# Kernel tuning notes

Measured on AMD Instinct MI355X. Metric: run time of the kernel, lower is better.

The kernel has to match this reference:

```python
import jax, jax.numpy as jnp
import numpy as np

SP = 4          # window/split size
HEADS = 8       # num_heads
SHIFTS = (0, 2) # shift_sizes


def _rel_pos_index(sp):
    # Same construction as the torch buffer `relative_position_index`.
    coords = np.stack(np.meshgrid(np.arange(sp), np.arange(sp), indexing='ij'))  # [2,sp,sp]
    coords = coords.reshape(2, -1)                                               # [2, sp*sp]
    rel = coords[:, :, None] - coords[:, None, :]                                # [2, N, N]
    rel = rel.transpose(1, 2, 0).astype(np.int64)                                # [N, N, 2]
    rel[..., 0] += sp - 1
    rel[..., 1] += sp - 1
    rel[..., 0] *= 2 * sp - 1
    return rel.sum(-1)  # [N, N]


def _window_attend(xh, qkv_w, lepe_w, bias, sp, heads, scale):
    # xh: [B, c, H, W] with c = split_dim
    B, c, H, W = xh.shape
    hd = c // heads
    h, w = H // sp, W // sp
    # 1x1 conv to qkv (no bias)
    qkv = jnp.einsum('oi,bihw->bohw', qkv_w, xh)
    q, k, v = jnp.split(qkv, 3, axis=1)
    # depthwise 3x3 LePE on v
    lepe = jax.lax.conv_general_dilated(v, lepe_w, (1, 1), 'SAME',
                                        feature_group_count=c)

    def part(t):
        # 'b (c head) (h hsp) (w wsp) -> (b h w) head (hsp wsp) c'
        t = t.reshape(B, hd, heads, h, sp, w, sp)
        t = t.transpose(0, 3, 5, 2, 4, 6, 1)  # b,h,w,head,hsp,wsp,hd
        return t.reshape(B * h * w, heads, sp * sp, hd)

    q, k, v, lepe = map(part, (q, k, v, lepe))
    attn = jnp.einsum('nhqc,nhkc->nhqk', q * scale, k) + bias[None]  # [N,heads,16,16]
    attn = jax.nn.softmax(attn, axis=-1)
    out = jnp.einsum('nhqk,nhkc->nhqc', attn, v) + lepe
    # inverse rearrange back to [B, c, H, W]
    out = out.reshape(B, h, w, heads, sp, sp, hd)
    out = out.transpose(0, 6, 3, 1, 4, 2, 5).reshape(B, c, H, W)
    return out


def setup_inputs() -> dict:
    key = jax.random.key(0)
    k1, k2, k3, k4 = jax.random.split(key, 4)
    x = jax.random.normal(k1, (8, 128, 192, 192), dtype=jnp.float32)
    qkv_w = jax.random.normal(k2, (192, 64), dtype=jnp.float32) * 0.05   # [3*split_dim, split_dim]
    lepe_w = jax.random.normal(k3, (64, 1, 3, 3), dtype=jnp.float32) * 0.05  # depthwise
    bias_table = jax.random.normal(k4, (49, 8), dtype=jnp.float32) * 0.02    # [(2sp-1)^2, heads]
    return {'x': x, 'qkv_w': qkv_w, 'lepe_w': lepe_w, 'bias_table': bias_table}


def reference(x, qkv_w, lepe_w, bias_table):
    B, C, H, W = x.shape
    c = C // 2
    hd = c // HEADS
    scale = hd ** -0.5
    idx = _rel_pos_index(SP)  # static numpy [16,16]
    bias = bias_table[idx.reshape(-1)].reshape(SP * SP, SP * SP, HEADS)
    bias = bias.transpose(2, 0, 1)  # [heads, 16, 16]

    results = []
    for s in SHIFTS:
        # NOTE: faithful to source, roll is over dims (1,2) = (channel, height)
        xs = jnp.roll(x, (-s, -s), axis=(1, 2)) if s > 0 else x
        halves = (xs[:, :c], xs[:, c:])
        outs = [_window_attend(xh, qkv_w, lepe_w, bias, SP, HEADS, scale)
                for xh in halves]
        if s > 0:
            outs = [jnp.roll(o, (s, s), axis=(1, 2)) for o in outs]
        results.append(jnp.concatenate(outs, axis=1))
    return results[0] + results[1]
```

## Files before the change

kernel.cpp:

```cpp
#include <hip/hip_runtime.h>

typedef __attribute__((ext_vector_type(8))) short short8v;
typedef __attribute__((ext_vector_type(8))) __fp16 h8v;
typedef __attribute__((ext_vector_type(2))) __fp16 h2v;
typedef __attribute__((ext_vector_type(4))) float f32x4;

__device__ inline unsigned short f2bf(float f) {
    unsigned u = __builtin_bit_cast(unsigned, f);
    return (unsigned short)((u + 0x7FFFu + ((u >> 16) & 1u)) >> 16);
}

__device__ inline float dot2(h2v a, h2v b, float c) {
#if __has_builtin(__builtin_amdgcn_fdot2)
    return __builtin_amdgcn_fdot2(a, b, c, false);
#else
    return c + (float)a[0] * (float)b[0] + (float)a[1] * (float)b[1];
#endif
}
__device__ inline h2v pk2h(float a, float b) {
#if __has_builtin(__builtin_amdgcn_cvt_pkrtz)
    return __builtin_bit_cast(h2v, __builtin_amdgcn_cvt_pkrtz(a, b));
#else
    h2v r; r[0] = (__fp16)a; r[1] = (__fp16)b; return r;
#endif
}

__global__ __launch_bounds__(256) void prep_weights(const float* __restrict__ qkv_w,
                                                    __fp16* __restrict__ wf) {
    int it = blockIdx.x * 256 + threadIdx.x;
    if (it >= 1536) return;
    int l = it & 63, frag = it >> 6;
    int which = frag >> 3, nt = (frag >> 1) & 3, kst = frag & 1;
    const float* src = qkv_w + (which * 64 + nt * 16 + (l & 15)) * 64 + kst * 32 + (l >> 4) * 8;
    h8v pk;
    #pragma unroll
    for (int j = 0; j < 8; ++j) pk[j] = (__fp16)src[j];
    *reinterpret_cast<h8v*>(wf + it * 8) = pk;
}

__global__ __launch_bounds__(256) void prep_x(const float* __restrict__ x,
                                              __fp16* __restrict__ xh) {
    const int xt = blockIdx.x;
    const int y  = blockIdx.y;
    const int b  = blockIdx.z;
    const int x0 = xt * 32;
    __shared__ float buf[128 * 33];

    for (int it = threadIdx.x; it < 1024; it += 256) {
        int c = it >> 3, xq = it & 7;
        const float4 v = *reinterpret_cast<const float4*>(
            x + ((b * 128 + c) * 192 + y) * 192 + x0 + xq * 4);
        float* d = &buf[c * 33 + xq * 4];
        d[0] = v.x; d[1] = v.y; d[2] = v.z; d[3] = v.w;
    }
    __syncthreads();

    for (int it = threadIdx.x; it < 512; it += 256) {
        int xl = it >> 4, c8 = it & 15;
        h8v pk;
        #pragma unroll
        for (int j = 0; j < 8; ++j) pk[j] = (__fp16)buf[(c8 * 8 + j) * 33 + xl];
        __fp16* dst = xh + (((size_t)(b * 192 + y) * 192) + x0 + xl) * 130 + c8 * 8;
        __builtin_memcpy(dst, &pk, 16);
    }
    if (threadIdx.x < 32) {
        int xl = threadIdx.x;
        h2v d2; d2[0] = (__fp16)buf[0 * 33 + xl]; d2[1] = (__fp16)buf[1 * 33 + xl];
        __fp16* dst = xh + (((size_t)(b * 192 + y) * 192) + x0 + xl) * 130 + 128;
        __builtin_memcpy(dst, &d2, 4);
    }
}

template<int SHIFT, bool ACCUM>
__global__ __launch_bounds__(256) void swin_main(
    const __fp16* __restrict__ xh,
    const __fp16* __restrict__ wfrag,
    const float* __restrict__ lepe_w,
    const float* __restrict__ bias_table,
    float* __restrict__ out)
{
    const int bx = blockIdx.x;
    const int wy = bx / 12, strip = bx % 12;
    const int half = blockIdx.y, b = blockIdx.z;
    const int tid = threadIdx.x;
    const int w = tid >> 6, l = tid & 63;

    __shared__ __fp16 xv[108 * 64];
    __shared__ __fp16 qs[64 * 64];
    __shared__ __fp16 ks[64 * 64];
    __shared__ __fp16 bias_s[392];
    __shared__ __fp16 lepe_s[576];

    for (int i = tid; i < 392; i += 256) bias_s[i] = (__fp16)bias_table[i];
    for (int i = tid; i < 576; i += 256) {
        int d = i & 7, rest = i >> 3;
        int j = rest % 9, h = rest / 9;
        lepe_s[i] = (__fp16)lepe_w[(d * 8 + h) * 9 + j];
    }

    const int ry0 = wy * 4 - 1, rx0 = strip * 16 - 1;
    for (int it = tid; it < 864; it += 256) {
        const int pos = it >> 3, slot = it & 7;
        const int py = pos / 18, px = pos - py * 18;
        const int ry = ry0 + py, rx = rx0 + px;
        h8v val;
        #pragma unroll
        for (int j = 0; j < 8; ++j) val[j] = (__fp16)0.f;
        if (ry >= 0 && ry < 192 && rx >= 0 && rx < 192) {
            int phys = ry + SHIFT; if (phys >= 192) phys -= 192;
            const int srcslot = slot ^ (pos & 7);
            const __fp16* src = xh + (((size_t)(b * 192 + phys) * 192) + rx) * 130
                                   + half * 64 + srcslot * 8 + SHIFT;
            __builtin_memcpy(&val, src, 16);
        }
        *reinterpret_cast<h8v*>(&xv[pos * 64 + slot * 8]) = val;
    }
    __syncthreads();

    const int tok16 = l & 15, g = l >> 4;
    h8v Aq[2], Av[3][2];
    {
        const int posq = (1 + (tok16 >> 2)) * 18 + w * 4 + 1 + (tok16 & 3);
        #pragma unroll
        for (int kst = 0; kst < 2; ++kst) {
            int chunk = (kst * 4 + g) ^ (posq & 7);
            Aq[kst] = *reinterpret_cast<const h8v*>(&xv[posq * 64 + chunk * 8]);
        }
        #pragma unroll
        for (int mt = 0; mt < 3; ++mt) {
            int t = mt * 16 + tok16;
            int posv = (t < 36) ? ((t / 6) * 18 + w * 4 + (t % 6)) : 0;
            #pragma unroll
            for (int kst = 0; kst < 2; ++kst) {
                int chunk = (kst * 4 + g) ^ (posv & 7);
                Av[mt][kst] = *reinterpret_cast<const h8v*>(&xv[posv * 64 + chunk * 8]);
            }
        }
    }
    __syncthreads();

    #pragma unroll
    for (int nt = 0; nt < 4; ++nt) {
        h8v Bq[2], Bk[2], Bv[2];
        #pragma unroll
        for (int kst = 0; kst < 2; ++kst) {
            Bq[kst] = *reinterpret_cast<const h8v*>(wfrag + (((0 * 8 + nt * 2 + kst) * 64 + l) * 8));
            Bk[kst] = *reinterpret_cast<const h8v*>(wfrag + (((1 * 8 + nt * 2 + kst) * 64 + l) * 8));
            Bv[kst] = *reinterpret_cast<const h8v*>(wfrag + (((2 * 8 + nt * 2 + kst) * 64 + l) * 8));
        }
        f32x4 aQ = {0.f,0.f,0.f,0.f}, aK = {0.f,0.f,0.f,0.f};
        f32x4 aV[3];
        #pragma unroll
        for (int mt = 0; mt < 3; ++mt) aV[mt] = (f32x4){0.f,0.f,0.f,0.f};
        #pragma unroll
        for (int kst = 0; kst < 2; ++kst) {
            aQ = __builtin_amdgcn_mfma_f32_16x16x32_f16(Aq[kst], Bq[kst], aQ, 0, 0, 0);
            aK = __builtin_amdgcn_mfma_f32_16x16x32_f16(Aq[kst], Bk[kst], aK, 0, 0, 0);
            #pragma unroll
            for (int mt = 0; mt < 3; ++mt)
                aV[mt] = __builtin_amdgcn_mfma_f32_16x16x32_f16(Av[mt][kst], Bv[kst], aV[mt], 0, 0, 0);
        }
        const int ch  = nt * 16 + tok16;
        const int chp = (ch & 7) * 8 + (ch >> 3);
        #pragma unroll
        for (int r = 0; r < 4; ++r) {
            const int qtok = w * 16 + 4 * g + r;
            const int pb = (((chp >> 3) ^ (qtok & 7)) * 8 + (chp & 7));
            qs[qtok * 64 + pb] = (__fp16)(aQ[r] * 0.35355339059327373f);
            ks[qtok * 64 + pb] = (__fp16)aK[r];
        }
        #pragma unroll
        for (int mt = 0; mt < 3; ++mt)
            #pragma unroll
            for (int r = 0; r < 4; ++r) {
                int t = mt * 16 + 4 * g + r;
                if (t < 36) {
                    int py = t / 6, px = t - py * 6;
                    int pos = py * 18 + w * 4 + px;
                    int pb = (((chp >> 3) ^ (pos & 7)) * 8 + (chp & 7));
                    xv[pos * 64 + pb] = (__fp16)aV[mt][r];
                }
            }
    }
    __syncthreads();

    {
        const int h = l >> 3, tqp = l & 7;
        const int qy0 = tqp >> 2, qx0 = tqp & 3;

        const int ox = strip * 16 + w * 4 + qx0;
        int oy0 = wy * 4 + qy0 + SHIFT;     if (oy0 >= 192) oy0 -= 192;
        int oy1 = wy * 4 + qy0 + 2 + SHIFT; if (oy1 >= 192) oy1 -= 192;
        int idx0[8], idx1[8];
        float prev0[8], prev1[8];
        #pragma unroll
        for (int d = 0; d < 8; ++d) {
            const int oc = half * 64 + ((d * 8 + h + SHIFT) & 63);
            idx0[d] = ((b * 128 + oc) * 192 + oy0) * 192 + ox;
            idx1[d] = ((b * 128 + oc) * 192 + oy1) * 192 + ox;
            if (ACCUM) { prev0[d] = out[idx0[d]]; prev1[d] = out[idx1[d]]; }
        }

        const int t0 = w * 16 + tqp, t1 = t0 + 8;
        h8v q0 = *reinterpret_cast<const h8v*>(&qs[t0 * 64 + (h ^ (t0 & 7)) * 8]);
        h8v q1 = *reinterpret_cast<const h8v*>(&qs[t1 * 64 + (h ^ (t1 & 7)) * 8]);
        const h2v* q0p = reinterpret_cast<const h2v*>(&q0);
        const h2v* q1p = reinterpret_cast<const h2v*>(&q1);

        float sc0[16], sc1[16];
        float den0 = 0.f, den1 = 0.f;
        #pragma unroll
        for (int tk = 0; tk < 16; ++tk) {
            const int kt = w * 16 + tk;
            h8v kr = *reinterpret_cast<const h8v*>(&ks[kt * 64 + (h ^ (kt & 7)) * 8]);
            const h2v* kp = reinterpret_cast<const h2v*>(&kr);
            float s0 = 0.f, s1 = 0.f;
            #pragma unroll
            for (int i = 0; i < 4; ++i) { s0 = dot2(q0p[i], kp[i], s0); s1 = dot2(q1p[i], kp[i], s1); }
            const int ky = tk >> 2, kx = tk & 3;
            s0 += (float)bias_s[((qy0 - ky + 3) * 7 + (qx0 - kx + 3)) * 8 + h];
            s1 += (float)bias_s[((qy0 + 2 - ky + 3) * 7 + (qx0 - kx + 3)) * 8 + h];
            s0 = __expf(s0); s1 = __expf(s1);
            sc0[tk] = s0; sc1[tk] = s1;
            den0 += s0; den1 += s1;
        }
        const float inv0 = 1.f / den0, inv1 = 1.f / den1;

        h2v o0pk[4], o1pk[4];
        #pragma unroll
        for (int j = 0; j < 4; ++j) { o0pk[j] = pk2h(0.f, 0.f); o1pk[j] = pk2h(0.f, 0.f); }
        #pragma unroll
        for (int tk = 0; tk < 16; ++tk) {
            const int pos = (1 + (tk >> 2)) * 18 + w * 4 + 1 + (tk & 3);
            h8v vr = *reinterpret_cast<const h8v*>(&xv[pos * 64 + (h ^ (pos & 7)) * 8]);
            const h2v* vp = reinterpret_cast<const h2v*>(&vr);
            const float f0 = sc0[tk] * inv0, f1 = sc1[tk] * inv1;
            const h2v pb0 = pk2h(f0, f0), pb1 = pk2h(f1, f1);
            #pragma unroll
            for (int j = 0; j < 4; ++j) {
                o0pk[j] += pb0 * vp[j];
                o1pk[j] += pb1 * vp[j];
            }
        }

        #pragma unroll
        for (int dy = 0; dy < 3; ++dy)
            #pragma unroll
            for (int dx = 0; dx < 3; ++dx) {
                int p0i = (qy0 + dy) * 18 + w * 4 + qx0 + dx;
                int p1i = p0i + 36;
                h8v v0 = *reinterpret_cast<const h8v*>(&xv[p0i * 64 + (h ^ (p0i & 7)) * 8]);
                h8v v1 = *reinterpret_cast<const h8v*>(&xv[p1i * 64 + (h ^ (p1i & 7)) * 8]);
                h8v lw = *reinterpret_cast<const h8v*>(&lepe_s[(h * 9 + dy * 3 + dx) * 8]);
                const h2v* v0p = reinterpret_cast<const h2v*>(&v0);
                const h2v* v1p = reinterpret_cast<const h2v*>(&v1);
                const h2v* lwp = reinterpret_cast<const h2v*>(&lw);
                #pragma unroll
                for (int j = 0; j < 4; ++j) {
                    o0pk[j] += v0p[j] * lwp[j];
                    o1pk[j] += v1p[j] * lwp[j];
                }
            }

        #pragma unroll
        for (int d = 0; d < 8; ++d) {
            const float a0 = (float)o0pk[d >> 1][d & 1];
            const float a1 = (float)o1pk[d >> 1][d & 1];
            if (ACCUM) { out[idx0[d]] = prev0[d] + a0; out[idx1[d]] = prev1[d] + a1; }
            else       { out[idx0[d]] = a0;            out[idx1[d]] = a1; }
        }
    }
}

template<int SHIFT, bool ACCUM>
__global__ __launch_bounds__(256) void swin_fb(
    const float* __restrict__ x, const float* __restrict__ qkv_w,
    const float* __restrict__ lepe_w, const float* __restrict__ bias_table,
    float* __restrict__ out)
{
    const int C = 128, HH = 192, WW = 192;
    const int win = blockIdx.x, wy = win / 48, wx = win % 48;
    const int half = blockIdx.y, b = blockIdx.z, tid = threadIdx.x;
    __shared__ short xpA[8 * 64 * 8];
    __shared__ float vs[64 * 37], qsf[64 * 17], ksf[64 * 17];
    __shared__ float bias_s[392], lepe_s[576];
    const int ys0 = wy * 4, xs0 = wx * 4;
    for (int i = tid; i < 392; i += 256) bias_s[i] = bias_table[i];
    for (int i = tid; i < 576; i += 256) lepe_s[i] = lepe_w[i];
    for (int item = tid; item < 512; item += 256) {
        const int slot = item >> 6, l = item & 63, kst = slot & 1;
        int p = 0; bool tvalid = true;
        if (slot < 6) { int t48 = (slot >> 1) * 16 + (l & 15); tvalid = (t48 < 36); p = t48; }
        else { int ti = l & 15; p = (1 + (ti >> 2)) * 6 + 1 + (ti & 3); }
        const int c0 = kst * 32 + (l >> 4) * 8;
        short8v pk;
        #pragma unroll
        for (int j = 0; j < 8; ++j) pk[j] = 0;
        if (tvalid) {
            int py = p / 6, px = p - py * 6;
            int ry = ys0 - 1 + py, rx = xs0 - 1 + px;
            if (ry >= 0 && ry < HH && rx >= 0 && rx < WW) {
                int oy = ry + SHIFT; if (oy >= HH) oy -= HH;
                #pragma unroll
                for (int j = 0; j < 8; ++j) {
                    int oc = half * 64 + c0 + j + SHIFT; if (oc >= C) oc -= C;
                    pk[j] = (short)f2bf(x[((b * C + oc) * HH + oy) * WW + rx]);
                }
            }
        }
        *reinterpret_cast<short8v*>(&xpA[item * 8]) = pk;
    }
    const int w = tid >> 6, l = tid & 63, nn = l & 15, g = l >> 4;
    short8v Bq[2], Bk[2], Bv[2];
    #pragma unroll
    for (int kst = 0; kst < 2; ++kst) {
        const int coff = kst * 32 + g * 8;
        const float* s0 = qkv_w + (w * 16 + nn) * 64 + coff;
        const float* s1 = qkv_w + (64 + w * 16 + nn) * 64 + coff;
        const float* s2 = qkv_w + (128 + w * 16 + nn) * 64 + coff;
        short8v p0, p1, p2;
        #pragma unroll
        for (int j = 0; j < 8; ++j) { p0[j] = (short)f2bf(s0[j]); p1[j] = (short)f2bf(s1[j]); p2[j] = (short)f2bf(s2[j]); }
        Bq[kst] = p0; Bk[kst] = p1; Bv[kst] = p2;
    }
    __syncthreads();
    {
        short8v Aq[2], Avf[3][2];
        #pragma unroll
        for (int kst = 0; kst < 2; ++kst)
            Aq[kst] = *reinterpret_cast<const short8v*>(&xpA[((6 + kst) * 64 + l) * 8]);
        #pragma unroll
        for (int mt = 0; mt < 3; ++mt)
            #pragma unroll
            for (int kst = 0; kst < 2; ++kst)
                Avf[mt][kst] = *reinterpret_cast<const short8v*>(&xpA[((mt * 2 + kst) * 64 + l) * 8]);
        f32x4 aQ = {0,0,0,0}, aK = {0,0,0,0}; f32x4 aV[3];
        #pragma unroll
        for (int mt = 0; mt < 3; ++mt) aV[mt] = (f32x4){0,0,0,0};
        #pragma unroll
        for (int kst = 0; kst < 2; ++kst) {
            aQ = __builtin_amdgcn_mfma_f32_16x16x32_bf16(Aq[kst], Bq[kst], aQ, 0, 0, 0);
            aK = __builtin_amdgcn_mfma_f32_16x16x32_bf16(Aq[kst], Bk[kst], aK, 0, 0, 0);
            #pragma unroll
            for (int mt = 0; mt < 3; ++mt)
                aV[mt] = __builtin_amdgcn_mfma_f32_16x16x32_bf16(Avf[mt][kst], Bv[kst], aV[mt], 0, 0, 0);
        }
        const int ch = w * 16 + nn;
        #pragma unroll
        for (int r = 0; r < 4; ++r) { qsf[ch * 17 + g * 4 + r] = aQ[r]; ksf[ch * 17 + g * 4 + r] = aK[r]; }
        #pragma unroll
        for (int mt = 0; mt < 3; ++mt)
            #pragma unroll
            for (int r = 0; r < 4; ++r) { int tok = mt * 16 + g * 4 + r; if (tok < 36) vs[ch * 37 + tok] = aV[mt][r]; }
    }
    __syncthreads();
    {
        const int tq = tid & 15, h = (tid >> 4) & 7, dh = tid >> 7;
        const int qy = tq >> 2, qx = tq & 3;
        const float scale = 0.35355339059327373f;
        float qreg[8];
        #pragma unroll
        for (int d = 0; d < 8; ++d) qreg[d] = qsf[(d * 8 + h) * 17 + tq] * scale;
        float sc[16]; float m = -1e30f;
        #pragma unroll
        for (int tk = 0; tk < 16; ++tk) {
            float s = 0.f;
            #pragma unroll
            for (int d = 0; d < 8; ++d) s += qreg[d] * ksf[(d * 8 + h) * 17 + tk];
            s += bias_s[((qy - (tk >> 2) + 3) * 7 + (qx - (tk & 3) + 3)) * 8 + h];
            sc[tk] = s; m = fmaxf(m, s);
        }
        float den = 0.f;
        #pragma unroll
        for (int tk = 0; tk < 16; ++tk) { sc[tk] = __expf(sc[tk] - m); den += sc[tk]; }
        const float inv = 1.f / den;
        float lw[4][9];
        #pragma unroll
        for (int dd = 0; dd < 4; ++dd) {
            int ch = (dh * 4 + dd) * 8 + h;
            #pragma unroll
            for (int j = 0; j < 9; ++j) lw[dd][j] = lepe_s[ch * 9 + j];
        }
        float o[4] = {0,0,0,0};
        #pragma unroll
        for (int tk = 0; tk < 16; ++tk) {
            int p = (1 + (tk >> 2)) * 6 + 1 + (tk & 3); float s = sc[tk];
            #pragma unroll
            for (int dd = 0; dd < 4; ++dd) o[dd] += s * vs[((dh * 4 + dd) * 8 + h) * 37 + p];
        }
        int oy = ys0 + qy + SHIFT; if (oy >= HH) oy -= HH;
        const int irx = xs0 + qx;
        #pragma unroll
        for (int dd = 0; dd < 4; ++dd) {
            const int ch = (dh * 4 + dd) * 8 + h;
            float val = o[dd] * inv;
            #pragma unroll
            for (int dy = 0; dy < 3; ++dy)
                #pragma unroll
                for (int dx = 0; dx < 3; ++dx)
                    val += vs[ch * 37 + (qy + dy) * 6 + (qx + dx)] * lw[dd][dy * 3 + dx];
            const int oc = half * 64 + ((ch + SHIFT) & 63);
            const int oidx = ((b * C + oc) * HH + oy) * WW + irx;
            if (ACCUM) out[oidx] += val; else out[oidx] = val;
        }
    }
}

extern "C" void kernel_launch(void* const* d_in, const int* in_sizes, int n_in,
                              void* d_out, int out_size, void* d_ws, size_t ws_size,
                              hipStream_t stream) {
    const float* x          = (const float*)d_in[0];
    const float* qkv_w      = (const float*)d_in[1];
    const float* lepe_w     = (const float*)d_in[2];
    const float* bias_table = (const float*)d_in[3];
    float* out = (float*)d_out;

    const size_t XH_BYTES = 8UL * 192 * 192 * 130 * 2;
    const size_t NEED = 32768 + XH_BYTES;

    if (ws_size >= NEED) {
        __fp16* wf = (__fp16*)d_ws;
        __fp16* xh = (__fp16*)((char*)d_ws + 32768);
        prep_weights<<<6, 256, 0, stream>>>(qkv_w, wf);
        prep_x<<<dim3(6, 192, 8), 256, 0, stream>>>(x, xh);
        dim3 grid(576, 2, 8);
        swin_main<0, false><<<grid, 256, 0, stream>>>(xh, wf, lepe_w, bias_table, out);
        swin_main<2, true ><<<grid, 256, 0, stream>>>(xh, wf, lepe_w, bias_table, out);
    } else {
        dim3 grid(48 * 48, 2, 8);
        swin_fb<0, false><<<grid, 256, 0, stream>>>(x, qkv_w, lepe_w, bias_table, out);
        swin_fb<2, true ><<<grid, 256, 0, stream>>>(x, qkv_w, lepe_w, bias_table, out);
    }
}
```

Baseline: 334.0 us.

## Pad fp16 staging stride, use exp2 softmax with packed scores, and relayout V pool

```diff
diff --git a/kernel.cpp b/kernel.cpp
--- a/kernel.cpp
+++ b/kernel.cpp
@@ -4,6 +4,8 @@
 typedef __attribute__((ext_vector_type(8))) __fp16 h8v;
 typedef __attribute__((ext_vector_type(2))) __fp16 h2v;
 typedef __attribute__((ext_vector_type(4))) float f32x4;
+
+#define XSTRIDE 136
 
 __device__ inline unsigned short f2bf(float f) {
     unsigned u = __builtin_bit_cast(unsigned, f);
@@ -22,6 +24,13 @@
     return __builtin_bit_cast(h2v, __builtin_amdgcn_cvt_pkrtz(a, b));
 #else
     h2v r; r[0] = (__fp16)a; r[1] = (__fp16)b; return r;
+#endif
+}
+__device__ inline float fexp2(float x) {
+#if __has_builtin(__builtin_amdgcn_exp2f)
+    return __builtin_amdgcn_exp2f(x);
+#else
+    return __expf(x * 0.6931471805599453f);
 #endif
 }
 
@@ -60,13 +69,13 @@
         h8v pk;
         #pragma unroll
         for (int j = 0; j < 8; ++j) pk[j] = (__fp16)buf[(c8 * 8 + j) * 33 + xl];
-        __fp16* dst = xh + (((size_t)(b * 192 + y) * 192) + x0 + xl) * 130 + c8 * 8;
+        __fp16* dst = xh + (((size_t)(b * 192 + y) * 192) + x0 + xl) * XSTRIDE + c8 * 8;
         __builtin_memcpy(dst, &pk, 16);
     }
     if (threadIdx.x < 32) {
         int xl = threadIdx.x;
         h2v d2; d2[0] = (__fp16)buf[0 * 33 + xl]; d2[1] = (__fp16)buf[1 * 33 + xl];
-        __fp16* dst = xh + (((size_t)(b * 192 + y) * 192) + x0 + xl) * 130 + 128;
+        __fp16* dst = xh + (((size_t)(b * 192 + y) * 192) + x0 + xl) * XSTRIDE + 128;
         __builtin_memcpy(dst, &d2, 4);
     }
 }
@@ -85,13 +94,13 @@
     const int tid = threadIdx.x;
     const int w = tid >> 6, l = tid & 63;
 
-    __shared__ __fp16 xv[108 * 64];
+    __shared__ __fp16 pool[9216];
     __shared__ __fp16 qs[64 * 64];
     __shared__ __fp16 ks[64 * 64];
-    __shared__ __fp16 bias_s[392];
+    __shared__ float  bias_s[392];
     __shared__ __fp16 lepe_s[576];
 
-    for (int i = tid; i < 392; i += 256) bias_s[i] = (__fp16)bias_table[i];
+    for (int i = tid; i < 392; i += 256) bias_s[i] = bias_table[i] * 1.4426950408889634f;
     for (int i = tid; i < 576; i += 256) {
         int d = i & 7, rest = i >> 3;
         int j = rest % 9, h = rest / 9;
@@ -109,11 +118,11 @@
         if (ry >= 0 && ry < 192 && rx >= 0 && rx < 192) {
             int phys = ry + SHIFT; if (phys >= 192) phys -= 192;
             const int srcslot = slot ^ (pos & 7);
-            const __fp16* src = xh + (((size_t)(b * 192 + phys) * 192) + rx) * 130
+            const __fp16* src = xh + (((size_t)(b * 192 + phys) * 192) + rx) * XSTRIDE
                                    + half * 64 + srcslot * 8 + SHIFT;
             __builtin_memcpy(&val, src, 16);
         }
-        *reinterpret_cast<h8v*>(&xv[pos * 64 + slot * 8]) = val;
+        *reinterpret_cast<h8v*>(&pool[pos * 64 + slot * 8]) = val;
     }
     __syncthreads();
 
@@ -124,7 +133,7 @@
         #pragma unroll
         for (int kst = 0; kst < 2; ++kst) {
             int chunk = (kst * 4 + g) ^ (posq & 7);
-            Aq[kst] = *reinterpret_cast<const h8v*>(&xv[posq * 64 + chunk * 8]);
+            Aq[kst] = *reinterpret_cast<const h8v*>(&pool[posq * 64 + chunk * 8]);
         }
         #pragma unroll
         for (int mt = 0; mt < 3; ++mt) {
@@ -133,7 +142,7 @@
             #pragma unroll
             for (int kst = 0; kst < 2; ++kst) {
                 int chunk = (kst * 4 + g) ^ (posv & 7);
-                Av[mt][kst] = *reinterpret_cast<const h8v*>(&xv[posv * 64 + chunk * 8]);
+                Av[mt][kst] = *reinterpret_cast<const h8v*>(&pool[posv * 64 + chunk * 8]);
             }
         }
     }
@@ -166,19 +175,17 @@
         for (int r = 0; r < 4; ++r) {
             const int qtok = w * 16 + 4 * g + r;
             const int pb = (((chp >> 3) ^ (qtok & 7)) * 8 + (chp & 7));
-            qs[qtok * 64 + pb] = (__fp16)(aQ[r] * 0.35355339059327373f);
+            qs[qtok * 64 + pb] = (__fp16)(aQ[r] * 0.5101293f);
             ks[qtok * 64 + pb] = (__fp16)aK[r];
         }
         #pragma unroll
         for (int mt = 0; mt < 3; ++mt)
             #pragma unroll
             for (int r = 0; r < 4; ++r) {
-                int t = mt * 16 + 4 * g + r;
+                const int t = mt * 16 + 4 * g + r;
                 if (t < 36) {
-                    int py = t / 6, px = t - py * 6;
-                    int pos = py * 18 + w * 4 + px;
-                    int pb = (((chp >> 3) ^ (pos & 7)) * 8 + (chp & 7));
-                    xv[pos * 64 + pb] = (__fp16)aV[mt][r];
+                    const int pb = (((chp >> 3) ^ (t & 7)) * 8 + (chp & 7));
+                    pool[(w * 36 + t) * 64 + pb] = (__fp16)aV[mt][r];
                 }
             }
     }
@@ -187,18 +194,19 @@
     {
         const int h = l >> 3, tqp = l & 7;
         const int qy0 = tqp >> 2, qx0 = tqp & 3;
+        const __fp16* vv = &pool[w * 36 * 64];
 
         const int ox = strip * 16 + w * 4 + qx0;
         int oy0 = wy * 4 + qy0 + SHIFT;     if (oy0 >= 192) oy0 -= 192;
         int oy1 = wy * 4 + qy0 + 2 + SHIFT; if (oy1 >= 192) oy1 -= 192;
-        int idx0[8], idx1[8];
+        const int ddelta = (oy1 - oy0) * 192;
+        int idx0[8];
         float prev0[8], prev1[8];
         #pragma unroll
         for (int d = 0; d < 8; ++d) {
             const int oc = half * 64 + ((d * 8 + h + SHIFT) & 63);
             idx0[d] = ((b * 128 + oc) * 192 + oy0) * 192 + ox;
-            idx1[d] = ((b * 128 + oc) * 192 + oy1) * 192 + ox;
-            if (ACCUM) { prev0[d] = out[idx0[d]]; prev1[d] = out[idx1[d]]; }
+            if (ACCUM) { prev0[d] = out[idx0[d]]; prev1[d] = out[idx0[d] + ddelta]; }
         }
 
         const int t0 = w * 16 + tqp, t1 = t0 + 8;
@@ -207,39 +215,52 @@
         const h2v* q0p = reinterpret_cast<const h2v*>(&q0);
         const h2v* q1p = reinterpret_cast<const h2v*>(&q1);
 
-        float sc0[16], sc1[16];
+        h2v scp0[8], scp1[8];
         float den0 = 0.f, den1 = 0.f;
         #pragma unroll
-        for (int tk = 0; tk < 16; ++tk) {
-            const int kt = w * 16 + tk;
-            h8v kr = *reinterpret_cast<const h8v*>(&ks[kt * 64 + (h ^ (kt & 7)) * 8]);
-            const h2v* kp = reinterpret_cast<const h2v*>(&kr);
-            float s0 = 0.f, s1 = 0.f;
-            #pragma unroll
-            for (int i = 0; i < 4; ++i) { s0 = dot2(q0p[i], kp[i], s0); s1 = dot2(q1p[i], kp[i], s1); }
-            const int ky = tk >> 2, kx = tk & 3;
-            s0 += (float)bias_s[((qy0 - ky + 3) * 7 + (qx0 - kx + 3)) * 8 + h];
-            s1 += (float)bias_s[((qy0 + 2 - ky + 3) * 7 + (qx0 - kx + 3)) * 8 + h];
-            s0 = __expf(s0); s1 = __expf(s1);
-            sc0[tk] = s0; sc1[tk] = s1;
-            den0 += s0; den1 += s1;
+        for (int tkp = 0; tkp < 8; ++tkp) {
+            float e0[2], e1[2];
+            #pragma unroll
+            for (int u = 0; u < 2; ++u) {
+                const int tk = tkp * 2 + u;
+                const int kt = w * 16 + tk;
+                h8v kr = *reinterpret_cast<const h8v*>(&ks[kt * 64 + (h ^ (kt & 7)) * 8]);
+                const h2v* kp = reinterpret_cast<const h2v*>(&kr);
+                float s0 = 0.f, s1 = 0.f;
+                #pragma unroll
+                for (int i = 0; i < 4; ++i) { s0 = dot2(q0p[i], kp[i], s0); s1 = dot2(q1p[i], kp[i], s1); }
+                const int ky = tk >> 2, kx = tk & 3;
+                s0 += bias_s[((qy0 - ky + 3) * 7 + (qx0 - kx + 3)) * 8 + h];
+                s1 += bias_s[((qy0 + 2 - ky + 3) * 7 + (qx0 - kx + 3)) * 8 + h];
+                e0[u] = fexp2(s0); e1[u] = fexp2(s1);
+            }
+            den0 += e0[0] + e0[1]; den1 += e1[0] + e1[1];
+            scp0[tkp] = pk2h(e0[0], e0[1]);
+            scp1[tkp] = pk2h(e1[0], e1[1]);
         }
         const float inv0 = 1.f / den0, inv1 = 1.f / den1;
+        const h2v ip0 = pk2h(inv0, inv0), ip1 = pk2h(inv1, inv1);
 
         h2v o0pk[4], o1pk[4];
         #pragma unroll
         for (int j = 0; j < 4; ++j) { o0pk[j] = pk2h(0.f, 0.f); o1pk[j] = pk2h(0.f, 0.f); }
         #pragma unroll
-        for (int tk = 0; tk < 16; ++tk) {
-            const int pos = (1 + (tk >> 2)) * 18 + w * 4 + 1 + (tk & 3);
-            h8v vr = *reinterpret_cast<const h8v*>(&xv[pos * 64 + (h ^ (pos & 7)) * 8]);
-            const h2v* vp = reinterpret_cast<const h2v*>(&vr);
-            const float f0 = sc0[tk] * inv0, f1 = sc1[tk] * inv1;
-            const h2v pb0 = pk2h(f0, f0), pb1 = pk2h(f1, f1);
-            #pragma unroll
-            for (int j = 0; j < 4; ++j) {
-                o0pk[j] += pb0 * vp[j];
-                o1pk[j] += pb1 * vp[j];
+        for (int tkp = 0; tkp < 8; ++tkp) {
+            const h2v w0 = scp0[tkp] * ip0;
+            const h2v w1 = scp1[tkp] * ip1;
+            #pragma unroll
+            for (int u = 0; u < 2; ++u) {
+                const int tk = tkp * 2 + u;
+                const int t = (1 + (tk >> 2)) * 6 + 1 + (tk & 3);
+                h8v vr = *reinterpret_cast<const h8v*>(&vv[t * 64 + (h ^ (t & 7)) * 8]);
+                const h2v* vp = reinterpret_cast<const h2v*>(&vr);
+                h2v b0; b0[0] = w0[u]; b0[1] = w0[u];
+                h2v b1; b1[0] = w1[u]; b1[1] = w1[u];
+                #pragma unroll
+                for (int j = 0; j < 4; ++j) {
+                    o0pk[j] += b0 * vp[j];
+                    o1pk[j] += b1 * vp[j];
+                }
             }
         }
 
@@ -247,10 +268,10 @@
         for (int dy = 0; dy < 3; ++dy)
             #pragma unroll
             for (int dx = 0; dx < 3; ++dx) {
-                int p0i = (qy0 + dy) * 18 + w * 4 + qx0 + dx;
-                int p1i = p0i + 36;
-                h8v v0 = *reinterpret_cast<const h8v*>(&xv[p0i * 64 + (h ^ (p0i & 7)) * 8]);
-                h8v v1 = *reinterpret_cast<const h8v*>(&xv[p1i * 64 + (h ^ (p1i & 7)) * 8]);
+                const int ta = (qy0 + dy) * 6 + qx0 + dx;
+                const int tb = ta + 12;
+                h8v v0 = *reinterpret_cast<const h8v*>(&vv[ta * 64 + (h ^ (ta & 7)) * 8]);
+                h8v v1 = *reinterpret_cast<const h8v*>(&vv[tb * 64 + (h ^ (tb & 7)) * 8]);
                 h8v lw = *reinterpret_cast<const h8v*>(&lepe_s[(h * 9 + dy * 3 + dx) * 8]);
                 const h2v* v0p = reinterpret_cast<const h2v*>(&v0);
                 const h2v* v1p = reinterpret_cast<const h2v*>(&v1);
@@ -266,8 +287,8 @@
         for (int d = 0; d < 8; ++d) {
             const float a0 = (float)o0pk[d >> 1][d & 1];
             const float a1 = (float)o1pk[d >> 1][d & 1];
-            if (ACCUM) { out[idx0[d]] = prev0[d] + a0; out[idx1[d]] = prev1[d] + a1; }
-            else       { out[idx0[d]] = a0;            out[idx1[d]] = a1; }
+            if (ACCUM) { out[idx0[d]] = prev0[d] + a0; out[idx0[d] + ddelta] = prev1[d] + a1; }
+            else       { out[idx0[d]] = a0;            out[idx0[d] + ddelta] = a1; }
         }
     }
 }
@@ -415,7 +436,7 @@
     const float* bias_table = (const float*)d_in[3];
     float* out = (float*)d_out;
 
-    const size_t XH_BYTES = 8UL * 192 * 192 * 130 * 2;
+    const size_t XH_BYTES = 8UL * 192 * 192 * XSTRIDE * 2;
     const size_t NEED = 32768 + XH_BYTES;
 
     if (ws_size >= NEED) {
```

After: 325.4 us. 1.03x faster.
